# Performance work log

Measured on AMD Instinct MI355X. Metric: run time of the kernel, lower is better.

The kernel has to match this reference:

```python
import jax, jax.numpy as jnp
import numpy as np

N_ORDER = 64
PRED_LEN = 720
SEQ_LEN = 720
ENC_IN = 321
BATCH = 16


def _hippo_legs(N):
    # HiPPO-LegS continuous transition (A, B), float64 numpy
    q = np.arange(N, dtype=np.float64)
    col, row = np.meshgrid(q, q)
    r = 2.0 * q + 1.0
    M = -(np.where(row >= col, r, 0.0) - np.diag(q))
    T = np.sqrt(np.diag(2.0 * q + 1.0))
    A = T @ M @ np.linalg.inv(T)
    B = np.diag(T)[:, None].copy()
    return A, B


def _discretize_bilinear(A, B, dt):
    # scipy.signal.cont2discrete(..., method='bilinear') equivalent
    N = A.shape[0]
    I = np.eye(N)
    BL = np.linalg.inv(I - (dt / 2.0) * A)
    Ad = BL @ (I + (dt / 2.0) * A)
    Bd = (BL @ (dt * B)).squeeze(-1)
    return Ad, Bd


def _legendre_eval_matrix(N, dt):
    # ss.eval_legendre(np.arange(N)[:,None], 1 - 2*vals).T via 3-term recurrence
    vals = np.arange(0.0, 1.0, dt)
    x = 1.0 - 2.0 * vals
    Ps = [np.ones_like(x), x]
    for n in range(1, N - 1):
        Ps.append(((2.0 * n + 1.0) * x * Ps[-1] - n * Ps[-2]) / (n + 1.0))
    return np.stack(Ps[:N], axis=0).T  # [len(vals), N]


def setup_inputs() -> dict:
    key = jax.random.key(0)
    k1, k2, k3 = jax.random.split(key, 3)
    dt = 1.0 / PRED_LEN
    A, B = _hippo_legs(N_ORDER)
    Ad, Bd = _discretize_bilinear(A, B, dt)
    eval_matrix = _legendre_eval_matrix(N_ORDER, dt)
    bound = 1.0 / np.sqrt(N_ORDER)  # torch nn.Linear default init range
    return {
        "x_enc": jax.random.normal(k1, (BATCH, SEQ_LEN, ENC_IN), dtype=jnp.float32),
        "A": jnp.asarray(Ad, dtype=jnp.float32),
        "B_vec": jnp.asarray(Bd, dtype=jnp.float32),
        "eval_matrix": jnp.asarray(eval_matrix, dtype=jnp.float32),
        "W_mlp": jax.random.uniform(k2, (N_ORDER, N_ORDER), jnp.float32, -bound, bound),
        "b_mlp": jax.random.uniform(k3, (N_ORDER,), jnp.float32, -bound, bound),
        "affine_weight": jnp.ones((1, 1, ENC_IN), jnp.float32),
        "affine_bias": jnp.zeros((1, 1, ENC_IN), jnp.float32),
    }


def reference(x_enc, A, B_vec, eval_matrix, W_mlp, b_mlp, affine_weight, affine_bias):
    P, N = eval_matrix.shape  # pred_len, proj_degree

    # RevIN-style instance normalization (means/stdev detached in torch)
    means = jax.lax.stop_gradient(jnp.mean(x_enc, axis=1, keepdims=True))
    x = x_enc - means
    stdev = jax.lax.stop_gradient(jnp.sqrt(jnp.var(x, axis=1, keepdims=True) + 1e-5))
    x = x / stdev
    x = x * affine_weight + affine_bias

    x_in = x[:, -P:]                         # [B, P, E]
    xs = jnp.transpose(x_in, (1, 0, 2))      # [P, B, E]: time-major for scan
    c0 = jnp.zeros((x_in.shape[0], x_in.shape[2], N), x_enc.dtype)

    def step(c, f):
        # c_t = c_{t-1} @ A^T + f_t B  (HiPPO-LegS linear recurrence)
        c_new = c @ A.T + f[..., None] * B_vec
        return c_new, c_new

    _, cs = jax.lax.scan(step, c0, xs)       # [P, B, E, N]

    out1 = cs @ W_mlp.T + b_mlp              # mlp over coefficient dim N
    x_dec_c = out1[P - 1]                    # [B, E, N] (seq_len >= pred_len branch)
    x_dec = x_dec_c @ eval_matrix.T          # [B, E, P] Legendre reconstruction
    x_dec = jnp.transpose(x_dec, (0, 2, 1))  # [B, P, E]

    # de-normalize
    x_dec = (x_dec - affine_bias) / (affine_weight + 1e-10)
    x_dec = x_dec * stdev + means
    return x_dec
```

## Files before the change

kernel.cpp:

```cpp
#include <hip/hip_runtime.h>
#include <math.h>

#define BATCH 16
#define SEQ   720
#define ENC   321
#define NORD  64
#define PRED  720
#define NPAIR (BATCH*ENC)

#define WS_KT    0
#define WS_EWT   (WS_KT + PRED*NORD)
#define WS_EVB   (WS_EWT + NORD*PRED)
#define WS_A16   (WS_EVB + PRED)
#define WS_KSUMP (WS_A16 + 4096)
#define WS_G     (WS_KSUMP + 17*64)
#define WS_PSUM  (WS_G + 4*96*4096)
#define WS_PSS   (WS_PSUM + 4*16*6*64)

#define MV4(AR, SVP, OUTV) do {                                                   \
    float _a0=0.f,_a1=0.f,_a2=0.f,_a3=0.f;                                        \
    _Pragma("unroll")                                                             \
    for (int _k = 0; _k < 4; _k++) {                                              \
        float4 _v0 = *(const float4*)&(SVP)[16*_k];                               \
        float4 _v1 = *(const float4*)&(SVP)[16*_k+4];                             \
        float4 _v2 = *(const float4*)&(SVP)[16*_k+8];                             \
        float4 _v3 = *(const float4*)&(SVP)[16*_k+12];                            \
        _a0 += (AR)[16*_k+0]*_v0.x + (AR)[16*_k+1]*_v0.y                          \
             + (AR)[16*_k+2]*_v0.z + (AR)[16*_k+3]*_v0.w;                         \
        _a1 += (AR)[16*_k+4]*_v1.x + (AR)[16*_k+5]*_v1.y                          \
             + (AR)[16*_k+6]*_v1.z + (AR)[16*_k+7]*_v1.w;                         \
        _a2 += (AR)[16*_k+8]*_v2.x + (AR)[16*_k+9]*_v2.y                          \
             + (AR)[16*_k+10]*_v2.z + (AR)[16*_k+11]*_v2.w;                       \
        _a3 += (AR)[16*_k+12]*_v3.x + (AR)[16*_k+13]*_v3.y                        \
             + (AR)[16*_k+14]*_v3.z + (AR)[16*_k+15]*_v3.w;                       \
    }                                                                             \
    OUTV = (_a0+_a1)+(_a2+_a3);                                                   \
} while (0)

__global__ __launch_bounds__(256, 1) void prep(const float* __restrict__ A,
        const float* __restrict__ Bv, float* __restrict__ ws)
{
    __shared__ float sv[4][64];
    const int tid  = threadIdx.x;
    const int lane = tid & 63;
    const int wv   = tid >> 6;
    if (blockIdx.x < 16) {
        float ar[64];
        #pragma unroll
        for (int k = 0; k < 16; k++) {
            float4 v = *(const float4*)&A[lane*64 + 4*k];
            ar[4*k]=v.x; ar[4*k+1]=v.y; ar[4*k+2]=v.z; ar[4*k+3]=v.w;
        }
        const int j = blockIdx.x*4 + wv;
        sv[wv][lane] = (lane == j) ? 1.f : 0.f;
        for (int s = 0; s < 16; s++) {
            float nv;
            MV4(ar, &sv[wv][0], nv);
            sv[wv][lane] = nv;
        }
        ws[WS_A16 + lane*64 + j] = sv[wv][lane];
    } else {
        if (tid >= 64) return;
        float ar[64];
        #pragma unroll
        for (int k = 0; k < 16; k++) {
            float4 v = *(const float4*)&A[lane*64 + 4*k];
            ar[4*k]=v.x; ar[4*k+1]=v.y; ar[4*k+2]=v.z; ar[4*k+3]=v.w;
        }
        float* Kt = ws + WS_KT;
        float bv = Bv[lane];
        sv[0][lane] = bv;
        Kt[(size_t)719*64 + lane] = bv;
        float ksml = bv;
        for (int j = 1; j <= 15; j++) {
            float nv;
            MV4(ar, &sv[0][0], nv);
            sv[0][lane] = nv;
            Kt[(size_t)(719 - j)*64 + lane] = nv;
            ksml += nv;
        }
        ws[WS_KSUMP + 16*64 + lane] = ksml;
    }
}

__global__ __launch_bounds__(256, 1) void chainsEW(const float* __restrict__ evalm,
        const float* __restrict__ W, const float* __restrict__ bm,
        float* __restrict__ ws)
{
    __shared__ float dsm[64*61];
    const int tid  = threadIdx.x;
    const int lane = tid & 63;
    const int wv   = tid >> 6;
    if (blockIdx.x < 16) {
        if (tid >= 64) return;
        float* sv = dsm;
        const int r = blockIdx.x;
        const float* A16 = ws + WS_A16;
        float* Kt = ws + WS_KT;
        float ar16[64];
        #pragma unroll
        for (int k = 0; k < 16; k++) {
            float4 v = *(const float4*)&A16[lane*64 + 4*k];
            ar16[4*k]=v.x; ar16[4*k+1]=v.y; ar16[4*k+2]=v.z; ar16[4*k+3]=v.w;
        }
        float ksml = 0.f;
        sv[lane] = Kt[(size_t)(719 - r)*64 + lane];
        for (int j = r + 16; j <= 719; j += 16) {
            float nv;
            MV4(ar16, sv, nv);
            sv[lane] = nv;
            Kt[(size_t)(719 - j)*64 + lane] = nv;
            ksml += nv;
        }
        ws[WS_KSUMP + r*64 + lane] = ksml;
    } else {
        float* Et = dsm;
        const int r = blockIdx.x - 16;
        float wcol[64];
        #pragma unroll
        for (int n = 0; n < 64; n++) wcol[n] = W[n*64 + lane];
        float bv = bm[lane];
        #pragma unroll
        for (int k = 0; k < 15; k++) {
            int row = wv + k*4;
            int tp = r*60 + row;
            const float* ev = evalm + (size_t)tp*64;
            float a0=0.f,a1=0.f,a2=0.f,a3=0.f;
            #pragma unroll
            for (int kk = 0; kk < 4; kk++) {
                float4 e0_ = *(const float4*)&ev[16*kk];
                float4 e1_ = *(const float4*)&ev[16*kk+4];
                float4 e2_ = *(const float4*)&ev[16*kk+8];
                float4 e3_ = *(const float4*)&ev[16*kk+12];
                a0 += e0_.x*wcol[16*kk+0] + e0_.y*wcol[16*kk+1]
                    + e0_.z*wcol[16*kk+2] + e0_.w*wcol[16*kk+3];
                a1 += e1_.x*wcol[16*kk+4] + e1_.y*wcol[16*kk+5]
                    + e1_.z*wcol[16*kk+6] + e1_.w*wcol[16*kk+7];
                a2 += e2_.x*wcol[16*kk+8] + e2_.y*wcol[16*kk+9]
                    + e2_.z*wcol[16*kk+10] + e2_.w*wcol[16*kk+11];
                a3 += e3_.x*wcol[16*kk+12] + e3_.y*wcol[16*kk+13]
                    + e3_.z*wcol[16*kk+14] + e3_.w*wcol[16*kk+15];
            }
            Et[lane*61 + row] = (a0+a1)+(a2+a3);
            float pv = ev[lane] * bv;
            #pragma unroll
            for (int o = 32; o > 0; o >>= 1) pv += __shfl_down(pv, o);
            if (lane == 0) ws[WS_EVB + tp] = pv;
        }
        __syncthreads();
        for (int idx = tid; idx < 4096; idx += 256) {
            int m = idx >> 6, row = idx & 63;
            if (row < 60)
                ws[WS_EWT + (size_t)m*720 + r*60 + row] = Et[m*61 + row];
        }
    }
}

__device__ inline float4 ldx(const float* __restrict__ x, int b, int t, int e4)
{
    float4 r = make_float4(0.f,0.f,0.f,0.f);
    const float* p = x + ((size_t)b*SEQ + t)*ENC;
    if (e4 + 3 < ENC) r = *(const float4*)&p[e4];
    else {
        if (e4   < ENC) r.x = p[e4];
        if (e4+1 < ENC) r.y = p[e4+1];
        if (e4+2 < ENC) r.z = p[e4+2];
    }
    return r;
}

__global__ __launch_bounds__(256) void k2(const float* __restrict__ x,
        float* __restrict__ ws)
{
    __shared__ float xt[2][12*64];
    __shared__ float ks[2][12*64];
    __shared__ float redn[12*64];
    __shared__ float reds[12*64];
    const int tid = threadIdx.x;
    const int bid = blockIdx.x;
    const int b = bid / 24, rem = bid % 24;
    const int et = rem / 4, tsp = rem % 4;
    const int e0 = et*64, t0 = tsp*180;

    const bool xon = tid < 192;
    const bool kon = tid >= 64;
    const int sx_t  = tid >> 4;
    const int sx_e4 = (tid & 15) * 4;
    const int sk    = tid - 64;
    const int sk_t  = sk >> 4;
    const int sk_m4 = (sk & 15) * 4;

    const float* Kt = ws + WS_KT;
    float s0=0,s1=0,s2=0,s3=0, q0=0,q1=0,q2=0,q3=0;
    float4 rx = make_float4(0,0,0,0), rk = make_float4(0,0,0,0);

    if (xon) rx = ldx(x, b, t0 + sx_t, e0 + sx_e4);
    if (kon) rk = *(const float4*)&Kt[(size_t)(t0 + sk_t)*64 + sk_m4];
    if (xon) {
        *(float4*)&xt[0][sx_t*64 + sx_e4] = rx;
        s0+=rx.x; s1+=rx.y; s2+=rx.z; s3+=rx.w;
        q0+=rx.x*rx.x; q1+=rx.y*rx.y; q2+=rx.z*rx.z; q3+=rx.w*rx.w;
    }
    if (kon) *(float4*)&ks[0][sk_t*64 + sk_m4] = rk;

    const bool con = tid < 128;
    const int elg = tid & 7;
    const int mgr = tid >> 3;
    float acc[8][4];
    #pragma unroll
    for (int j = 0; j < 8; j++)
        #pragma unroll
        for (int i = 0; i < 4; i++) acc[j][i] = 0.f;

    for (int ch = 0; ch < 15; ch++) {
        if (ch + 1 < 15) {
            if (xon) rx = ldx(x, b, t0 + (ch+1)*12 + sx_t, e0 + sx_e4);
            if (kon) rk = *(const float4*)&Kt[(size_t)(t0 + (ch+1)*12 + sk_t)*64 + sk_m4];
        }
        __syncthreads();
        const float* xb = xt[ch & 1];
        const float* kb = ks[ch & 1];
        if (con) {
            #pragma unroll
            for (int tt = 0; tt < 12; tt++) {
                float4 fa = *(const float4*)&xb[tt*64 + elg*8];
                float4 fb = *(const float4*)&xb[tt*64 + elg*8 + 4];
                float4 kv = *(const float4*)&kb[tt*64 + mgr*4];
                acc[0][0]+=fa.x*kv.x; acc[0][1]+=fa.x*kv.y; acc[0][2]+=fa.x*kv.z; acc[0][3]+=fa.x*kv.w;
                acc[1][0]+=fa.y*kv.x; acc[1][1]+=fa.y*kv.y; acc[1][2]+=fa.y*kv.z; acc[1][3]+=fa.y*kv.w;
                acc[2][0]+=fa.z*kv.x; acc[2][1]+=fa.z*kv.y; acc[2][2]+=fa.z*kv.z; acc[2][3]+=fa.z*kv.w;
                acc[3][0]+=fa.w*kv.x; acc[3][1]+=fa.w*kv.y; acc[3][2]+=fa.w*kv.z; acc[3][3]+=fa.w*kv.w;
                acc[4][0]+=fb.x*kv.x; acc[4][1]+=fb.x*kv.y; acc[4][2]+=fb.x*kv.z; acc[4][3]+=fb.x*kv.w;
                acc[5][0]+=fb.y*kv.x; acc[5][1]+=fb.y*kv.y; acc[5][2]+=fb.y*kv.z; acc[5][3]+=fb.y*kv.w;
                acc[6][0]+=fb.z*kv.x; acc[6][1]+=fb.z*kv.y; acc[6][2]+=fb.z*kv.z; acc[6][3]+=fb.z*kv.w;
                acc[7][0]+=fb.w*kv.x; acc[7][1]+=fb.w*kv.y; acc[7][2]+=fb.w*kv.z; acc[7][3]+=fb.w*kv.w;
            }
        }
        if (ch + 1 < 15) {
            if (xon) {
                *(float4*)&xt[(ch+1)&1][sx_t*64 + sx_e4] = rx;
                s0+=rx.x; s1+=rx.y; s2+=rx.z; s3+=rx.w;
                q0+=rx.x*rx.x; q1+=rx.y*rx.y; q2+=rx.z*rx.z; q3+=rx.w*rx.w;
            }
            if (kon) *(float4*)&ks[(ch+1)&1][sk_t*64 + sk_m4] = rk;
        }
    }

    if (con) {
        float* g = ws + WS_G + (size_t)(tsp*96 + b*6 + et)*4096;
        #pragma unroll
        for (int i = 0; i < 4; i++) {
            float* gr = g + (mgr*4 + i)*64 + elg*8;
            *(float4*)&gr[0] = make_float4(acc[0][i], acc[1][i], acc[2][i], acc[3][i]);
            *(float4*)&gr[4] = make_float4(acc[4][i], acc[5][i], acc[6][i], acc[7][i]);
        }
    }

    __syncthreads();
    if (xon) {
        redn[sx_t*64 + sx_e4+0] = s0; redn[sx_t*64 + sx_e4+1] = s1;
        redn[sx_t*64 + sx_e4+2] = s2; redn[sx_t*64 + sx_e4+3] = s3;
        reds[sx_t*64 + sx_e4+0] = q0; reds[sx_t*64 + sx_e4+1] = q1;
        reds[sx_t*64 + sx_e4+2] = q2; reds[sx_t*64 + sx_e4+3] = q3;
    }
    __syncthreads();
    if (tid < 64) {
        float s = 0.f, q = 0.f;
        #pragma unroll
        for (int rr = 0; rr < 12; rr++) { s += redn[rr*64 + tid]; q += reds[rr*64 + tid]; }
        const size_t o = (size_t)((tsp*16 + b)*6 + et)*64 + tid;
        ws[WS_PSUM + o] = s;
        ws[WS_PSS  + o] = q;
    }
}

#define K3ROW(r, wvv) \
    acc[r][0]+=(wvv)*c0.x; acc[r][1]+=(wvv)*c0.y; acc[r][2]+=(wvv)*c0.z; acc[r][3]+=(wvv)*c0.w; \
    acc[r][4]+=(wvv)*c1.x; acc[r][5]+=(wvv)*c1.y; acc[r][6]+=(wvv)*c1.z; acc[r][7]+=(wvv)*c1.w;

__global__ __launch_bounds__(256) void k3f(const float* __restrict__ aw,
        const float* __restrict__ ab, const float* __restrict__ ws,
        float* __restrict__ out)
{
    __shared__ float Cm[64*192];
    __shared__ float EWm[64*196];
    __shared__ float ssc[128], ssh[128], sP[128], sQ[128];
    __shared__ float kss[64];
    const int tid = threadIdx.x;
    const int b   = blockIdx.x / 12;
    const int rr  = blockIdx.x % 12;
    const int eT  = rr >> 2;
    const int tq  = rr & 3;
    const int e0  = eT * 128;
    const int et0 = eT * 2;

    if (tid < 128) {
        const int el = tid, e = e0 + el;
        const int et = et0 + (el >> 6), eli = el & 63;
        float s = 0.f, q = 0.f;
        #pragma unroll
        for (int tsp = 0; tsp < 4; tsp++) {
            const size_t o = (size_t)((tsp*16 + b)*6 + et)*64 + eli;
            s += ws[WS_PSUM + o];
            q += ws[WS_PSS  + o];
        }
        float mean = s * (1.0f/SEQ);
        float var  = q * (1.0f/SEQ) - mean*mean;
        float sd   = sqrtf(var + 1e-5f);
        if (e < ENC) {
            float a = aw[e], av = ab[e];
            float sc = a / sd;
            float P  = sd / (a + 1e-10f);
            ssc[el] = sc; ssh[el] = av - mean*sc;
            sP[el]  = P;  sQ[el]  = mean - av*P;
        } else {
            ssc[el]=0.f; ssh[el]=0.f; sP[el]=0.f; sQ[el]=0.f;
        }
    }
    if (tid < 64) {
        float s = 0.f;
        #pragma unroll
        for (int p = 0; p < 17; p++) s += ws[WS_KSUMP + p*64 + tid];
        kss[tid] = s;
    }
    __syncthreads();

    const float* G = ws + WS_G;
    #pragma unroll
    for (int k = 0; k < 8; k++) {
        int slot = k*256 + tid;
        int m = slot >> 5, el4 = (slot & 31) * 4;
        int et = et0 + (el4 >> 6), eli4 = el4 & 63;
        size_t base = (size_t)(b*6 + et)*4096 + m*64 + eli4;
        float4 g0 = *(const float4*)&G[base];
        float4 g1 = *(const float4*)&G[base + (size_t) 96*4096];
        float4 g2 = *(const float4*)&G[base + (size_t)192*4096];
        float4 g3 = *(const float4*)&G[base + (size_t)288*4096];
        float km = kss[m];
        float4 sc = *(const float4*)&ssc[el4];
        float4 sh = *(const float4*)&ssh[el4];
        float4 c;
        c.x = sc.x*(g0.x+g1.x+g2.x+g3.x) + sh.x*km;
        c.y = sc.y*(g0.y+g1.y+g2.y+g3.y) + sh.y*km;
        c.z = sc.z*(g0.z+g1.z+g2.z+g3.z) + sh.z*km;
        c.w = sc.w*(g0.w+g1.w+g2.w+g3.w) + sh.w*km;
        *(float4*)&Cm[m*192 + (el4>>3)*12 + (el4&7)] = c;
    }

    const float* EWT = ws + WS_EWT;
    #pragma unroll
    for (int it = 0; it < 12; it++) {
        int slot = it*256 + tid;
        int m = slot / 48, t4 = (slot % 48) * 4;
        int tp = tq*192 + t4;
        float4 v;
        if (tp + 3 < PRED) v = *(const float4*)&EWT[(size_t)m*720 + tp];
        else {
            v = make_float4(0.f,0.f,0.f,0.f);
            if (tp   < PRED) v.x = EWT[(size_t)m*720 + tp];
            if (tp+1 < PRED) v.y = EWT[(size_t)m*720 + tp+1];
            if (tp+2 < PRED) v.z = EWT[(size_t)m*720 + tp+2];
        }
        *(float4*)&EWm[m*196 + t4] = v;
    }
    __syncthreads();

    const int tx = tid & 15;
    const int ty = tid >> 4;
    float acc[12][8];
    #pragma unroll
    for (int r = 0; r < 12; r++)
        #pragma unroll
        for (int j = 0; j < 8; j++) acc[r][j] = 0.f;

    const float* cb = Cm  + tx*12;
    const float* wb = EWm + ty*12;
    #pragma unroll 2
    for (int m = 0; m < 64; m++) {
        float4 c0 = *(const float4*)&cb[m*192];
        float4 c1 = *(const float4*)&cb[m*192 + 4];
        float4 w0 = *(const float4*)&wb[m*196];
        float4 w1 = *(const float4*)&wb[m*196 + 4];
        float4 w2 = *(const float4*)&wb[m*196 + 8];
        K3ROW(0,  w0.x) K3ROW(1,  w0.y) K3ROW(2,  w0.z) K3ROW(3,  w0.w)
        K3ROW(4,  w1.x) K3ROW(5,  w1.y) K3ROW(6,  w1.z) K3ROW(7,  w1.w)
        K3ROW(8,  w2.x) K3ROW(9,  w2.y) K3ROW(10, w2.z) K3ROW(11, w2.w)
    }

    const int elb = tx*8;
    const int eb  = e0 + elb;
    float4 Pa = *(const float4*)&sP[elb];
    float4 Pb = *(const float4*)&sP[elb+4];
    float4 Qa = *(const float4*)&sQ[elb];
    float4 Qb = *(const float4*)&sQ[elb+4];
    const float* evb = ws + WS_EVB;
    #pragma unroll
    for (int r = 0; r < 12; r++) {
        int tp = tq*192 + ty*12 + r;
        if (tp < PRED) {
            float ev = evb[tp];
            float* op = out + ((size_t)b*PRED + tp)*ENC;
            if (eb + 7 < ENC) {
                float4 o0, o1;
                o0.x = (acc[r][0]+ev)*Pa.x + Qa.x;
                o0.y = (acc[r][1]+ev)*Pa.y + Qa.y;
                o0.z = (acc[r][2]+ev)*Pa.z + Qa.z;
                o0.w = (acc[r][3]+ev)*Pa.w + Qa.w;
                o1.x = (acc[r][4]+ev)*Pb.x + Qb.x;
                o1.y = (acc[r][5]+ev)*Pb.y + Qb.y;
                o1.z = (acc[r][6]+ev)*Pb.z + Qb.z;
                o1.w = (acc[r][7]+ev)*Pb.w + Qb.w;
                *(float4*)&op[eb]   = o0;
                *(float4*)&op[eb+4] = o1;
            } else {
                if (eb   < ENC) op[eb  ] = (acc[r][0]+ev)*Pa.x + Qa.x;
                if (eb+1 < ENC) op[eb+1] = (acc[r][1]+ev)*Pa.y + Qa.y;
                if (eb+2 < ENC) op[eb+2] = (acc[r][2]+ev)*Pa.z + Qa.z;
                if (eb+3 < ENC) op[eb+3] = (acc[r][3]+ev)*Pa.w + Qa.w;
                if (eb+4 < ENC) op[eb+4] = (acc[r][4]+ev)*Pb.x + Qb.x;
                if (eb+5 < ENC) op[eb+5] = (acc[r][5]+ev)*Pb.y + Qb.y;
                if (eb+6 < ENC) op[eb+6] = (acc[r][6]+ev)*Pb.z + Qb.z;
                if (eb+7 < ENC) op[eb+7] = (acc[r][7]+ev)*Pb.w + Qb.w;
            }
        }
    }
}

extern "C" void kernel_launch(void* const* d_in, const int* in_sizes, int n_in,
                              void* d_out, int out_size, void* d_ws, size_t ws_size,
                              hipStream_t stream)
{
    const float* x     = (const float*)d_in[0];
    const float* A     = (const float*)d_in[1];
    const float* Bv    = (const float*)d_in[2];
    const float* evalm = (const float*)d_in[3];
    const float* W     = (const float*)d_in[4];
    const float* bm    = (const float*)d_in[5];
    const float* aw    = (const float*)d_in[6];
    const float* ab    = (const float*)d_in[7];
    float* ws  = (float*)d_ws;
    float* out = (float*)d_out;

    prep    <<<17, 256, 0, stream>>>(A, Bv, ws);
    chainsEW<<<28, 256, 0, stream>>>(evalm, W, bm, ws);
    k2      <<<BATCH*6*4, 256, 0, stream>>>(x, ws);
    k3f     <<<192, 256, 0, stream>>>(aw, ab, ws, out);
}
```

Measured before the change: 148.9 us.

## Shorten serial kernel chains with A^64 stride and split time slabs finer

The sequential power chain computing the kernel rows K_t is restructured: A^64 is formed from A^16, 16 seeds are extended with A^16 to 64 seeds, and 64 independent chains then stride by 64. This cuts the longest serial dependency from about 45 steps to about 11, at the cost of one more kernel launch and extra workspace. Separately, the main reduction kernel now splits time into 8 slabs of 90 instead of 4 of 180, doubling the block count for better GPU occupancy. The final kernel must then sum 8 partial G slabs, adding memory traffic.

```diff
diff --git a/kernel.cpp b/kernel.cpp
--- a/kernel.cpp
+++ b/kernel.cpp
@@ -6,16 +6,21 @@
 #define ENC   321
 #define NORD  64
 #define PRED  720
-#define NPAIR (BATCH*ENC)
+
+#define NSLAB 8
+#define TSLAB 90
+#define TCH   10
+#define NCH   9
 
 #define WS_KT    0
 #define WS_EWT   (WS_KT + PRED*NORD)
 #define WS_EVB   (WS_EWT + NORD*PRED)
 #define WS_A16   (WS_EVB + PRED)
-#define WS_KSUMP (WS_A16 + 4096)
-#define WS_G     (WS_KSUMP + 17*64)
-#define WS_PSUM  (WS_G + 4*96*4096)
-#define WS_PSS   (WS_PSUM + 4*16*6*64)
+#define WS_A64   (WS_A16 + 4096)
+#define WS_KSUMP (WS_A64 + 4096)
+#define WS_G     (WS_KSUMP + 81*64)
+#define WS_PSUM  (WS_G + NSLAB*96*4096)
+#define WS_PSS   (WS_PSUM + NSLAB*16*6*64)
 
 #define MV4(AR, SVP, OUTV) do {                                                   \
     float _a0=0.f,_a1=0.f,_a2=0.f,_a3=0.f;                                        \
@@ -79,11 +84,11 @@
             Kt[(size_t)(719 - j)*64 + lane] = nv;
             ksml += nv;
         }
-        ws[WS_KSUMP + 16*64 + lane] = ksml;
-    }
-}
-
-__global__ __launch_bounds__(256, 1) void chainsEW(const float* __restrict__ evalm,
+        ws[WS_KSUMP + 80*64 + lane] = ksml;
+    }
+}
+
+__global__ __launch_bounds__(256, 1) void mid(const float* __restrict__ evalm,
         const float* __restrict__ W, const float* __restrict__ bm,
         float* __restrict__ ws)
 {
@@ -92,30 +97,48 @@
     const int lane = tid & 63;
     const int wv   = tid >> 6;
     if (blockIdx.x < 16) {
-        if (tid >= 64) return;
-        float* sv = dsm;
-        const int r = blockIdx.x;
         const float* A16 = ws + WS_A16;
-        float* Kt = ws + WS_KT;
-        float ar16[64];
+        float ar[64];
         #pragma unroll
         for (int k = 0; k < 16; k++) {
             float4 v = *(const float4*)&A16[lane*64 + 4*k];
-            ar16[4*k]=v.x; ar16[4*k+1]=v.y; ar16[4*k+2]=v.z; ar16[4*k+3]=v.w;
-        }
+            ar[4*k]=v.x; ar[4*k+1]=v.y; ar[4*k+2]=v.z; ar[4*k+3]=v.w;
+        }
+        const int j = blockIdx.x*4 + wv;
+        float* sv = dsm + wv*64;
+        sv[lane] = (lane == j) ? 1.f : 0.f;
+        #pragma unroll
+        for (int s = 0; s < 4; s++) {
+            float nv;
+            MV4(ar, sv, nv);
+            sv[lane] = nv;
+        }
+        ws[WS_A64 + lane*64 + j] = sv[lane];
+    } else if (blockIdx.x < 20) {
+        const float* A16 = ws + WS_A16;
+        float ar[64];
+        #pragma unroll
+        for (int k = 0; k < 16; k++) {
+            float4 v = *(const float4*)&A16[lane*64 + 4*k];
+            ar[4*k]=v.x; ar[4*k+1]=v.y; ar[4*k+2]=v.z; ar[4*k+3]=v.w;
+        }
+        const int r = (blockIdx.x - 16)*4 + wv;
+        float* Kt = ws + WS_KT;
+        float* sv = dsm + wv*64;
+        sv[lane] = Kt[(size_t)(719 - r)*64 + lane];
         float ksml = 0.f;
-        sv[lane] = Kt[(size_t)(719 - r)*64 + lane];
-        for (int j = r + 16; j <= 719; j += 16) {
+        #pragma unroll
+        for (int s = 1; s <= 3; s++) {
             float nv;
-            MV4(ar16, sv, nv);
+            MV4(ar, sv, nv);
             sv[lane] = nv;
-            Kt[(size_t)(719 - j)*64 + lane] = nv;
+            Kt[(size_t)(719 - (r + 16*s))*64 + lane] = nv;
             ksml += nv;
         }
-        ws[WS_KSUMP + r*64 + lane] = ksml;
+        ws[WS_KSUMP + (64 + r)*64 + lane] = ksml;
     } else {
         float* Et = dsm;
-        const int r = blockIdx.x - 16;
+        const int r = blockIdx.x - 20;
         float wcol[64];
         #pragma unroll
         for (int n = 0; n < 64; n++) wcol[n] = W[n*64 + lane];
@@ -156,6 +179,34 @@
     }
 }
 
+__global__ __launch_bounds__(256, 1) void chains64(float* __restrict__ ws)
+{
+    __shared__ float svb[4][64];
+    const int tid  = threadIdx.x;
+    const int lane = tid & 63;
+    const int wv   = tid >> 6;
+    const int r    = blockIdx.x*4 + wv;
+    const float* A64 = ws + WS_A64;
+    float* Kt = ws + WS_KT;
+    float ar[64];
+    #pragma unroll
+    for (int k = 0; k < 16; k++) {
+        float4 v = *(const float4*)&A64[lane*64 + 4*k];
+        ar[4*k]=v.x; ar[4*k+1]=v.y; ar[4*k+2]=v.z; ar[4*k+3]=v.w;
+    }
+    float* sv = svb[wv];
+    sv[lane] = Kt[(size_t)(719 - r)*64 + lane];
+    float ksml = 0.f;
+    for (int j = r + 64; j <= 719; j += 64) {
+        float nv;
+        MV4(ar, sv, nv);
+        sv[lane] = nv;
+        Kt[(size_t)(719 - j)*64 + lane] = nv;
+        ksml += nv;
+    }
+    ws[WS_KSUMP + r*64 + lane] = ksml;
+}
+
 __device__ inline float4 ldx(const float* __restrict__ x, int b, int t, int e4)
 {
     float4 r = make_float4(0.f,0.f,0.f,0.f);
@@ -172,21 +223,21 @@
 __global__ __launch_bounds__(256) void k2(const float* __restrict__ x,
         float* __restrict__ ws)
 {
-    __shared__ float xt[2][12*64];
-    __shared__ float ks[2][12*64];
-    __shared__ float redn[12*64];
-    __shared__ float reds[12*64];
+    __shared__ float xt[2][TCH*64];
+    __shared__ float ks[2][TCH*64];
+    __shared__ float redn[TCH*64];
+    __shared__ float reds[TCH*64];
     const int tid = threadIdx.x;
     const int bid = blockIdx.x;
-    const int b = bid / 24, rem = bid % 24;
-    const int et = rem / 4, tsp = rem % 4;
-    const int e0 = et*64, t0 = tsp*180;
-
-    const bool xon = tid < 192;
-    const bool kon = tid >= 64;
+    const int b = bid / 48, rem = bid % 48;
+    const int et = rem >> 3, tsp = rem & 7;
+    const int e0 = et*64, t0 = tsp*TSLAB;
+
+    const bool xon = tid < 16*TCH;
+    const bool kon = tid >= 256 - 16*TCH;
     const int sx_t  = tid >> 4;
     const int sx_e4 = (tid & 15) * 4;
-    const int sk    = tid - 64;
+    const int sk    = tid - (256 - 16*TCH);
     const int sk_t  = sk >> 4;
     const int sk_m4 = (sk & 15) * 4;
 
@@ -212,17 +263,17 @@
         #pragma unroll
         for (int i = 0; i < 4; i++) acc[j][i] = 0.f;
 
-    for (int ch = 0; ch < 15; ch++) {
-        if (ch + 1 < 15) {
-            if (xon) rx = ldx(x, b, t0 + (ch+1)*12 + sx_t, e0 + sx_e4);
-            if (kon) rk = *(const float4*)&Kt[(size_t)(t0 + (ch+1)*12 + sk_t)*64 + sk_m4];
+    for (int ch = 0; ch < NCH; ch++) {
+        if (ch + 1 < NCH) {
+            if (xon) rx = ldx(x, b, t0 + (ch+1)*TCH + sx_t, e0 + sx_e4);
+            if (kon) rk = *(const float4*)&Kt[(size_t)(t0 + (ch+1)*TCH + sk_t)*64 + sk_m4];
         }
         __syncthreads();
         const float* xb = xt[ch & 1];
         const float* kb = ks[ch & 1];
         if (con) {
             #pragma unroll
-            for (int tt = 0; tt < 12; tt++) {
+            for (int tt = 0; tt < TCH; tt++) {
                 float4 fa = *(const float4*)&xb[tt*64 + elg*8];
                 float4 fb = *(const float4*)&xb[tt*64 + elg*8 + 4];
                 float4 kv = *(const float4*)&kb[tt*64 + mgr*4];
@@ -236,7 +287,7 @@
                 acc[7][0]+=fb.w*kv.x; acc[7][1]+=fb.w*kv.y; acc[7][2]+=fb.w*kv.z; acc[7][3]+=fb.w*kv.w;
             }
         }
-        if (ch + 1 < 15) {
+        if (ch + 1 < NCH) {
             if (xon) {
                 *(float4*)&xt[(ch+1)&1][sx_t*64 + sx_e4] = rx;
                 s0+=rx.x; s1+=rx.y; s2+=rx.z; s3+=rx.w;
@@ -267,7 +318,7 @@
     if (tid < 64) {
         float s = 0.f, q = 0.f;
         #pragma unroll
-        for (int rr = 0; rr < 12; rr++) { s += redn[rr*64 + tid]; q += reds[rr*64 + tid]; }
+        for (int rr = 0; rr < TCH; rr++) { s += redn[rr*64 + tid]; q += reds[rr*64 + tid]; }
         const size_t o = (size_t)((tsp*16 + b)*6 + et)*64 + tid;
         ws[WS_PSUM + o] = s;
         ws[WS_PSS  + o] = q;
@@ -299,7 +350,7 @@
         const int et = et0 + (el >> 6), eli = el & 63;
         float s = 0.f, q = 0.f;
         #pragma unroll
-        for (int tsp = 0; tsp < 4; tsp++) {
+        for (int tsp = 0; tsp < NSLAB; tsp++) {
             const size_t o = (size_t)((tsp*16 + b)*6 + et)*64 + eli;
             s += ws[WS_PSUM + o];
             q += ws[WS_PSS  + o];
@@ -319,8 +370,7 @@
     }
     if (tid < 64) {
         float s = 0.f;
-        #pragma unroll
-        for (int p = 0; p < 17; p++) s += ws[WS_KSUMP + p*64 + tid];
+        for (int p = 0; p < 81; p++) s += ws[WS_KSUMP + p*64 + tid];
         kss[tid] = s;
     }
     __syncthreads();
@@ -332,18 +382,20 @@
         int m = slot >> 5, el4 = (slot & 31) * 4;
         int et = et0 + (el4 >> 6), eli4 = el4 & 63;
         size_t base = (size_t)(b*6 + et)*4096 + m*64 + eli4;
-        float4 g0 = *(const float4*)&G[base];
-        float4 g1 = *(const float4*)&G[base + (size_t) 96*4096];
-        float4 g2 = *(const float4*)&G[base + (size_t)192*4096];
-        float4 g3 = *(const float4*)&G[base + (size_t)288*4096];
+        float4 gs = make_float4(0.f,0.f,0.f,0.f);
+        #pragma unroll
+        for (int s2 = 0; s2 < NSLAB; s2++) {
+            float4 gv = *(const float4*)&G[base + (size_t)s2*96*4096];
+            gs.x += gv.x; gs.y += gv.y; gs.z += gv.z; gs.w += gv.w;
+        }
         float km = kss[m];
         float4 sc = *(const float4*)&ssc[el4];
         float4 sh = *(const float4*)&ssh[el4];
         float4 c;
-        c.x = sc.x*(g0.x+g1.x+g2.x+g3.x) + sh.x*km;
-        c.y = sc.y*(g0.y+g1.y+g2.y+g3.y) + sh.y*km;
-        c.z = sc.z*(g0.z+g1.z+g2.z+g3.z) + sh.z*km;
-        c.w = sc.w*(g0.w+g1.w+g2.w+g3.w) + sh.w*km;
+        c.x = sc.x*gs.x + sh.x*km;
+        c.y = sc.y*gs.y + sh.y*km;
+        c.z = sc.z*gs.z + sh.z*km;
+        c.w = sc.w*gs.w + sh.w*km;
         *(float4*)&Cm[m*192 + (el4>>3)*12 + (el4&7)] = c;
     }
 
@@ -442,7 +494,8 @@
     float* out = (float*)d_out;
 
     prep    <<<17, 256, 0, stream>>>(A, Bv, ws);
-    chainsEW<<<28, 256, 0, stream>>>(evalm, W, bm, ws);
-    k2      <<<BATCH*6*4, 256, 0, stream>>>(x, ws);
+    mid     <<<32, 256, 0, stream>>>(evalm, W, bm, ws);
+    chains64<<<16, 256, 0, stream>>>(ws);
+    k2      <<<16*6*NSLAB, 256, 0, stream>>>(x, ws);
     k3f     <<<192, 256, 0, stream>>>(aw, ab, ws, out);
 }
```

Result: slower. 154.0 us (+3.4%).

## Shorten HiPPO kernel-power chain via A^64 stride and cooperative head kernel

Applied to the files above, without the earlier changes.

The serial chain computing the impulse-response vectors K_t was split into 16 chains of about 45 dependent mat-vec steps using A^16. The new code also computes A^64 and seeds 64 chains, each running about 11 steps, which shortens the critical serial path. The three setup phases are fused into one cooperative kernel with grid syncs, replacing separate launches, and there is a multi-kernel fallback if the cooperative launch fails. In exchange it adds an extra A^64 matrix-power pass, grid-sync overhead, and a longer partial-sum reduction (81 rows) in k2.

```diff
diff --git a/kernel.cpp b/kernel.cpp
--- a/kernel.cpp
+++ b/kernel.cpp
@@ -1,19 +1,22 @@
 #include <hip/hip_runtime.h>
+#include <hip/hip_cooperative_groups.h>
 #include <math.h>
+
+namespace cg = cooperative_groups;
 
 #define BATCH 16
 #define SEQ   720
 #define ENC   321
 #define NORD  64
 #define PRED  720
-#define NPAIR (BATCH*ENC)
 
 #define WS_KT    0
 #define WS_EWT   (WS_KT + PRED*NORD)
 #define WS_EVB   (WS_EWT + NORD*PRED)
 #define WS_A16   (WS_EVB + PRED)
-#define WS_KSUMP (WS_A16 + 4096)
-#define WS_G     (WS_KSUMP + 17*64)
+#define WS_A64   (WS_A16 + 4096)
+#define WS_KSUMP (WS_A64 + 4096)
+#define WS_G     (WS_KSUMP + 81*64)
 #define WS_PSUM  (WS_G + 4*96*4096)
 #define WS_PSS   (WS_PSUM + 4*16*6*64)
 
@@ -37,85 +40,57 @@
     OUTV = (_a0+_a1)+(_a2+_a3);                                                   \
 } while (0)
 
-__global__ __launch_bounds__(256, 1) void prep(const float* __restrict__ A,
-        const float* __restrict__ Bv, float* __restrict__ ws)
-{
-    __shared__ float sv[4][64];
+#define LOADROW(AR, SRC) do {                                                     \
+    _Pragma("unroll")                                                             \
+    for (int _k = 0; _k < 16; _k++) {                                             \
+        float4 _v = *(const float4*)&(SRC)[lane*64 + 4*_k];                       \
+        (AR)[4*_k]=_v.x; (AR)[4*_k+1]=_v.y; (AR)[4*_k+2]=_v.z; (AR)[4*_k+3]=_v.w; \
+    }                                                                             \
+} while (0)
+
+__device__ __forceinline__ void head_phase1(const float* __restrict__ A,
+        const float* __restrict__ Bv, const float* __restrict__ evalm,
+        const float* __restrict__ W, const float* __restrict__ bm,
+        float* __restrict__ ws, float* dsm)
+{
     const int tid  = threadIdx.x;
     const int lane = tid & 63;
     const int wv   = tid >> 6;
-    if (blockIdx.x < 16) {
+    const int bid  = blockIdx.x;
+    if (bid < 16) {
         float ar[64];
-        #pragma unroll
-        for (int k = 0; k < 16; k++) {
-            float4 v = *(const float4*)&A[lane*64 + 4*k];
-            ar[4*k]=v.x; ar[4*k+1]=v.y; ar[4*k+2]=v.z; ar[4*k+3]=v.w;
-        }
-        const int j = blockIdx.x*4 + wv;
-        sv[wv][lane] = (lane == j) ? 1.f : 0.f;
+        LOADROW(ar, A);
+        const int j = bid*4 + wv;
+        float* sv = dsm + wv*64;
+        sv[lane] = (lane == j) ? 1.f : 0.f;
         for (int s = 0; s < 16; s++) {
             float nv;
-            MV4(ar, &sv[wv][0], nv);
-            sv[wv][lane] = nv;
-        }
-        ws[WS_A16 + lane*64 + j] = sv[wv][lane];
-    } else {
-        if (tid >= 64) return;
-        float ar[64];
-        #pragma unroll
-        for (int k = 0; k < 16; k++) {
-            float4 v = *(const float4*)&A[lane*64 + 4*k];
-            ar[4*k]=v.x; ar[4*k+1]=v.y; ar[4*k+2]=v.z; ar[4*k+3]=v.w;
-        }
-        float* Kt = ws + WS_KT;
-        float bv = Bv[lane];
-        sv[0][lane] = bv;
-        Kt[(size_t)719*64 + lane] = bv;
-        float ksml = bv;
-        for (int j = 1; j <= 15; j++) {
-            float nv;
-            MV4(ar, &sv[0][0], nv);
-            sv[0][lane] = nv;
-            Kt[(size_t)(719 - j)*64 + lane] = nv;
-            ksml += nv;
-        }
-        ws[WS_KSUMP + 16*64 + lane] = ksml;
-    }
-}
-
-__global__ __launch_bounds__(256, 1) void chainsEW(const float* __restrict__ evalm,
-        const float* __restrict__ W, const float* __restrict__ bm,
-        float* __restrict__ ws)
-{
-    __shared__ float dsm[64*61];
-    const int tid  = threadIdx.x;
-    const int lane = tid & 63;
-    const int wv   = tid >> 6;
-    if (blockIdx.x < 16) {
-        if (tid >= 64) return;
-        float* sv = dsm;
-        const int r = blockIdx.x;
-        const float* A16 = ws + WS_A16;
-        float* Kt = ws + WS_KT;
-        float ar16[64];
-        #pragma unroll
-        for (int k = 0; k < 16; k++) {
-            float4 v = *(const float4*)&A16[lane*64 + 4*k];
-            ar16[4*k]=v.x; ar16[4*k+1]=v.y; ar16[4*k+2]=v.z; ar16[4*k+3]=v.w;
-        }
-        float ksml = 0.f;
-        sv[lane] = Kt[(size_t)(719 - r)*64 + lane];
-        for (int j = r + 16; j <= 719; j += 16) {
-            float nv;
-            MV4(ar16, sv, nv);
+            MV4(ar, sv, nv);
             sv[lane] = nv;
-            Kt[(size_t)(719 - j)*64 + lane] = nv;
-            ksml += nv;
-        }
-        ws[WS_KSUMP + r*64 + lane] = ksml;
+        }
+        ws[WS_A16 + lane*64 + j] = sv[lane];
+    } else if (bid == 16) {
+        if (tid < 64) {
+            float ar[64];
+            LOADROW(ar, A);
+            float* Kt = ws + WS_KT;
+            float bv = Bv[lane];
+            float* sv = dsm;
+            sv[lane] = bv;
+            Kt[(size_t)719*64 + lane] = bv;
+            float ksml = bv;
+            for (int j = 1; j <= 15; j++) {
+                float nv;
+                MV4(ar, sv, nv);
+                sv[lane] = nv;
+                Kt[(size_t)(719 - j)*64 + lane] = nv;
+                ksml += nv;
+            }
+            ws[WS_KSUMP + 80*64 + lane] = ksml;
+        }
     } else {
         float* Et = dsm;
-        const int r = blockIdx.x - 16;
+        const int r = bid - 17;
         float wcol[64];
         #pragma unroll
         for (int n = 0; n < 64; n++) wcol[n] = W[n*64 + lane];
@@ -156,6 +131,97 @@
     }
 }
 
+__device__ __forceinline__ void head_phase2(float* __restrict__ ws, float* dsm)
+{
+    const int tid  = threadIdx.x;
+    const int lane = tid & 63;
+    const int wv   = tid >> 6;
+    const int bid  = blockIdx.x;
+    if (bid < 16) {
+        const float* A16 = ws + WS_A16;
+        float ar[64];
+        LOADROW(ar, A16);
+        const int j = bid*4 + wv;
+        float* sv = dsm + wv*64;
+        sv[lane] = (lane == j) ? 1.f : 0.f;
+        #pragma unroll
+        for (int s = 0; s < 4; s++) {
+            float nv;
+            MV4(ar, sv, nv);
+            sv[lane] = nv;
+        }
+        ws[WS_A64 + lane*64 + j] = sv[lane];
+    } else if (bid < 20) {
+        const float* A16 = ws + WS_A16;
+        float ar[64];
+        LOADROW(ar, A16);
+        const int r = (bid - 16)*4 + wv;
+        float* Kt = ws + WS_KT;
+        float* sv = dsm + wv*64;
+        sv[lane] = Kt[(size_t)(719 - r)*64 + lane];
+        float ksml = 0.f;
+        #pragma unroll
+        for (int s = 1; s <= 3; s++) {
+            float nv;
+            MV4(ar, sv, nv);
+            sv[lane] = nv;
+            Kt[(size_t)(719 - (r + 16*s))*64 + lane] = nv;
+            ksml += nv;
+        }
+        ws[WS_KSUMP + (64 + r)*64 + lane] = ksml;
+    }
+}
+
+__device__ __forceinline__ void head_phase3(float* __restrict__ ws, float* dsm)
+{
+    const int tid  = threadIdx.x;
+    const int lane = tid & 63;
+    const int wv   = tid >> 6;
+    const int bid  = blockIdx.x;
+    if (bid < 16) {
+        const float* A64 = ws + WS_A64;
+        float ar[64];
+        LOADROW(ar, A64);
+        const int r = bid*4 + wv;
+        float* Kt = ws + WS_KT;
+        float* sv = dsm + wv*64;
+        sv[lane] = Kt[(size_t)(719 - r)*64 + lane];
+        float ksml = 0.f;
+        for (int j = r + 64; j <= 719; j += 64) {
+            float nv;
+            MV4(ar, sv, nv);
+            sv[lane] = nv;
+            Kt[(size_t)(719 - j)*64 + lane] = nv;
+            ksml += nv;
+        }
+        ws[WS_KSUMP + r*64 + lane] = ksml;
+    }
+}
+
+__global__ __launch_bounds__(256, 1) void head_coop(const float* __restrict__ A,
+        const float* __restrict__ Bv, const float* __restrict__ evalm,
+        const float* __restrict__ W, const float* __restrict__ bm,
+        float* __restrict__ ws)
+{
+    __shared__ float dsm[64*61];
+    cg::grid_group g = cg::this_grid();
+    head_phase1(A, Bv, evalm, W, bm, ws, dsm);
+    g.sync();
+    head_phase2(ws, dsm);
+    g.sync();
+    head_phase3(ws, dsm);
+}
+
+__global__ __launch_bounds__(256, 1) void head_p1(const float* __restrict__ A,
+        const float* __restrict__ Bv, const float* __restrict__ evalm,
+        const float* __restrict__ W, const float* __restrict__ bm,
+        float* __restrict__ ws)
+{ __shared__ float dsm[64*61]; head_phase1(A, Bv, evalm, W, bm, ws, dsm); }
+__global__ __launch_bounds__(256, 1) void head_p2(float* __restrict__ ws)
+{ __shared__ float dsm[64*61]; head_phase2(ws, dsm); }
+__global__ __launch_bounds__(256, 1) void head_p3(float* __restrict__ ws)
+{ __shared__ float dsm[64*61]; head_phase3(ws, dsm); }
+
 __device__ inline float4 ldx(const float* __restrict__ x, int b, int t, int e4)
 {
     float4 r = make_float4(0.f,0.f,0.f,0.f);
@@ -319,8 +385,7 @@
     }
     if (tid < 64) {
         float s = 0.f;
-        #pragma unroll
-        for (int p = 0; p < 17; p++) s += ws[WS_KSUMP + p*64 + tid];
+        for (int p = 0; p < 81; p++) s += ws[WS_KSUMP + p*64 + tid];
         kss[tid] = s;
     }
     __syncthreads();
@@ -441,8 +506,15 @@
     float* ws  = (float*)d_ws;
     float* out = (float*)d_out;
 
-    prep    <<<17, 256, 0, stream>>>(A, Bv, ws);
-    chainsEW<<<28, 256, 0, stream>>>(evalm, W, bm, ws);
-    k2      <<<BATCH*6*4, 256, 0, stream>>>(x, ws);
-    k3f     <<<192, 256, 0, stream>>>(aw, ab, ws, out);
-}
+    void* hargs[6] = {(void*)&A, (void*)&Bv, (void*)&evalm,
+                      (void*)&W, (void*)&bm, (void*)&ws};
+    hipError_t ce = hipLaunchCooperativeKernel((void*)head_coop, dim3(29), dim3(256),
+                                               hargs, 0, stream);
+    if (ce != hipSuccess) {
+        head_p1<<<29, 256, 0, stream>>>(A, Bv, evalm, W, bm, ws);
+        head_p2<<<20, 256, 0, stream>>>(ws);
+        head_p3<<<16, 256, 0, stream>>>(ws);
+    }
+    k2 <<<BATCH*6*4, 256, 0, stream>>>(x, ws);
+    k3f<<<192, 256, 0, stream>>>(aw, ab, ws, out);
+}
```

Measured after the change: 192.8 us. 1.29x slower.

## Use all 256 threads for k2 outer product and read K directly from global

Applied to the files above, without the earlier changes.

The k2 kernel's 64x64 outer-product accumulation now runs on all 256 threads, each holding a 4x4 tile, instead of 128 threads with 8x4 tiles. The shared-memory staging of the K matrix is removed, and each thread reads its K float4 straight from global memory (likely L2/cache-resident). This raises compute parallelism and lowers register pressure and LDS use per block. In exchange it adds global-load latency inside the inner loop, since those K reads are no longer prefetched.

```diff
diff --git a/kernel.cpp b/kernel.cpp
--- a/kernel.cpp
+++ b/kernel.cpp
@@ -173,7 +173,6 @@
         float* __restrict__ ws)
 {
     __shared__ float xt[2][12*64];
-    __shared__ float ks[2][12*64];
     __shared__ float redn[12*64];
     __shared__ float reds[12*64];
     const int tid = threadIdx.x;
@@ -183,78 +182,55 @@
     const int e0 = et*64, t0 = tsp*180;
 
     const bool xon = tid < 192;
-    const bool kon = tid >= 64;
     const int sx_t  = tid >> 4;
     const int sx_e4 = (tid & 15) * 4;
-    const int sk    = tid - 64;
-    const int sk_t  = sk >> 4;
-    const int sk_m4 = (sk & 15) * 4;
 
     const float* Kt = ws + WS_KT;
     float s0=0,s1=0,s2=0,s3=0, q0=0,q1=0,q2=0,q3=0;
-    float4 rx = make_float4(0,0,0,0), rk = make_float4(0,0,0,0);
-
-    if (xon) rx = ldx(x, b, t0 + sx_t, e0 + sx_e4);
-    if (kon) rk = *(const float4*)&Kt[(size_t)(t0 + sk_t)*64 + sk_m4];
+    float4 rx = make_float4(0,0,0,0);
+
     if (xon) {
+        rx = ldx(x, b, t0 + sx_t, e0 + sx_e4);
         *(float4*)&xt[0][sx_t*64 + sx_e4] = rx;
         s0+=rx.x; s1+=rx.y; s2+=rx.z; s3+=rx.w;
         q0+=rx.x*rx.x; q1+=rx.y*rx.y; q2+=rx.z*rx.z; q3+=rx.w*rx.w;
     }
-    if (kon) *(float4*)&ks[0][sk_t*64 + sk_m4] = rk;
-
-    const bool con = tid < 128;
-    const int elg = tid & 7;
-    const int mgr = tid >> 3;
-    float acc[8][4];
-    #pragma unroll
-    for (int j = 0; j < 8; j++)
+
+    const int elg = tid & 15;
+    const int mgr = tid >> 4;
+    float acc[4][4];
+    #pragma unroll
+    for (int j = 0; j < 4; j++)
         #pragma unroll
         for (int i = 0; i < 4; i++) acc[j][i] = 0.f;
 
     for (int ch = 0; ch < 15; ch++) {
-        if (ch + 1 < 15) {
-            if (xon) rx = ldx(x, b, t0 + (ch+1)*12 + sx_t, e0 + sx_e4);
-            if (kon) rk = *(const float4*)&Kt[(size_t)(t0 + (ch+1)*12 + sk_t)*64 + sk_m4];
-        }
+        if (ch + 1 < 15 && xon)
+            rx = ldx(x, b, t0 + (ch+1)*12 + sx_t, e0 + sx_e4);
         __syncthreads();
         const float* xb = xt[ch & 1];
-        const float* kb = ks[ch & 1];
-        if (con) {
-            #pragma unroll
-            for (int tt = 0; tt < 12; tt++) {
-                float4 fa = *(const float4*)&xb[tt*64 + elg*8];
-                float4 fb = *(const float4*)&xb[tt*64 + elg*8 + 4];
-                float4 kv = *(const float4*)&kb[tt*64 + mgr*4];
-                acc[0][0]+=fa.x*kv.x; acc[0][1]+=fa.x*kv.y; acc[0][2]+=fa.x*kv.z; acc[0][3]+=fa.x*kv.w;
-                acc[1][0]+=fa.y*kv.x; acc[1][1]+=fa.y*kv.y; acc[1][2]+=fa.y*kv.z; acc[1][3]+=fa.y*kv.w;
-                acc[2][0]+=fa.z*kv.x; acc[2][1]+=fa.z*kv.y; acc[2][2]+=fa.z*kv.z; acc[2][3]+=fa.z*kv.w;
-                acc[3][0]+=fa.w*kv.x; acc[3][1]+=fa.w*kv.y; acc[3][2]+=fa.w*kv.z; acc[3][3]+=fa.w*kv.w;
-                acc[4][0]+=fb.x*kv.x; acc[4][1]+=fb.x*kv.y; acc[4][2]+=fb.x*kv.z; acc[4][3]+=fb.x*kv.w;
-                acc[5][0]+=fb.y*kv.x; acc[5][1]+=fb.y*kv.y; acc[5][2]+=fb.y*kv.z; acc[5][3]+=fb.y*kv.w;
-                acc[6][0]+=fb.z*kv.x; acc[6][1]+=fb.z*kv.y; acc[6][2]+=fb.z*kv.z; acc[6][3]+=fb.z*kv.w;
-                acc[7][0]+=fb.w*kv.x; acc[7][1]+=fb.w*kv.y; acc[7][2]+=fb.w*kv.z; acc[7][3]+=fb.w*kv.w;
-            }
-        }
-        if (ch + 1 < 15) {
-            if (xon) {
-                *(float4*)&xt[(ch+1)&1][sx_t*64 + sx_e4] = rx;
-                s0+=rx.x; s1+=rx.y; s2+=rx.z; s3+=rx.w;
-                q0+=rx.x*rx.x; q1+=rx.y*rx.y; q2+=rx.z*rx.z; q3+=rx.w*rx.w;
-            }
-            if (kon) *(float4*)&ks[(ch+1)&1][sk_t*64 + sk_m4] = rk;
-        }
-    }
-
-    if (con) {
-        float* g = ws + WS_G + (size_t)(tsp*96 + b*6 + et)*4096;
-        #pragma unroll
-        for (int i = 0; i < 4; i++) {
-            float* gr = g + (mgr*4 + i)*64 + elg*8;
-            *(float4*)&gr[0] = make_float4(acc[0][i], acc[1][i], acc[2][i], acc[3][i]);
-            *(float4*)&gr[4] = make_float4(acc[4][i], acc[5][i], acc[6][i], acc[7][i]);
-        }
-    }
+        const float* kp = Kt + (size_t)(t0 + ch*12)*64 + mgr*4;
+        #pragma unroll
+        for (int tt = 0; tt < 12; tt++) {
+            float4 fa = *(const float4*)&xb[tt*64 + elg*4];
+            float4 kv = *(const float4*)&kp[tt*64];
+            acc[0][0]+=fa.x*kv.x; acc[0][1]+=fa.x*kv.y; acc[0][2]+=fa.x*kv.z; acc[0][3]+=fa.x*kv.w;
+            acc[1][0]+=fa.y*kv.x; acc[1][1]+=fa.y*kv.y; acc[1][2]+=fa.y*kv.z; acc[1][3]+=fa.y*kv.w;
+            acc[2][0]+=fa.z*kv.x; acc[2][1]+=fa.z*kv.y; acc[2][2]+=fa.z*kv.z; acc[2][3]+=fa.z*kv.w;
+            acc[3][0]+=fa.w*kv.x; acc[3][1]+=fa.w*kv.y; acc[3][2]+=fa.w*kv.z; acc[3][3]+=fa.w*kv.w;
+        }
+        if (ch + 1 < 15 && xon) {
+            *(float4*)&xt[(ch+1)&1][sx_t*64 + sx_e4] = rx;
+            s0+=rx.x; s1+=rx.y; s2+=rx.z; s3+=rx.w;
+            q0+=rx.x*rx.x; q1+=rx.y*rx.y; q2+=rx.z*rx.z; q3+=rx.w*rx.w;
+        }
+    }
+
+    float* g = ws + WS_G + (size_t)(tsp*96 + b*6 + et)*4096;
+    #pragma unroll
+    for (int i = 0; i < 4; i++)
+        *(float4*)&g[(mgr*4 + i)*64 + elg*4] =
+            make_float4(acc[0][i], acc[1][i], acc[2][i], acc[3][i]);
 
     __syncthreads();
     if (xon) {
```

Measured after the change: 144.1 us (median of 2 runs). 1.03x faster.
